# Kernel optimization log

Measured on AMD Instinct MI355X. Metric: run time of the kernel, lower is better.

Reference implementation:

```python
import jax, jax.numpy as jnp
import numpy as np

B, T, N, DIN, D = 8, 20, 1000, 64, 64


def setup_inputs() -> dict:
    key = jax.random.key(0)
    ks = jax.random.split(key, 10)
    stdv = 1.0 / np.sqrt(DIN + D)  # torch reset_param: uniform(-1/sqrt(in_size), ...)
    def gate_w(k):
        return jax.random.uniform(k, (N, DIN + D, D), jnp.float32, -stdv, stdv)
    x = jax.random.normal(ks[0], (B, T, N, DIN), jnp.float32)
    # xavier_normal_ for time_att.W [N, T, D]: fan_in=T*D, fan_out=N*D
    xav_std = np.sqrt(2.0 / (T * D + N * D)).astype(np.float32)
    Wt = jax.random.normal(ks[5], (N, T, D), jnp.float32) * xav_std
    return {
        "x": x,
        "Wi": gate_w(ks[1]), "bi": jnp.zeros((N, D), jnp.float32),
        "Wo": gate_w(ks[2]), "bo": jnp.zeros((N, D), jnp.float32),
        "Wf": gate_w(ks[3]), "bf": jnp.zeros((N, D), jnp.float32),
        "Wc": gate_w(ks[4]), "bc": jnp.zeros((N, D), jnp.float32),
        "Wt": Wt,
    }


def _lstm_att(x, Wi, bi, Wo, bo, Wf, bf, Wc, bc, Wt):
    b, t, n, din = x.shape
    d = Wi.shape[-1]

    def gate(xh, W, bias):
        # per-stock matmul: [b,n,din+d] x [n,din+d,d] -> [b,n,d]
        return jnp.einsum('bni,nio->bno', xh, W) + bias

    def step(carry, xt):
        h, c = carry  # [b,n,d]
        xh = jnp.concatenate([xt, h], axis=-1)
        it = jax.nn.sigmoid(gate(xh, Wi, bi))
        ot = jax.nn.sigmoid(gate(xh, Wo, bo))
        ft = jax.nn.sigmoid(gate(xh, Wf, bf))
        ch = jnp.tanh(gate(xh, Wc, bc))
        c2 = ft * c + it * ch
        h2 = ot * jnp.tanh(c2)
        return (h2, c2), h2

    h0 = jnp.zeros((b, n, d), x.dtype)
    c0 = jnp.zeros((b, n, d), x.dtype)
    xt_seq = jnp.swapaxes(x, 0, 1)  # [t,b,n,din]
    _, hs = jax.lax.scan(step, (h0, c0), xt_seq)
    h = jnp.swapaxes(hs, 0, 1)  # [b,t,n,d] (torch.stack dim=-3)

    # time attention
    h_bntd = jnp.swapaxes(h, 1, 2)  # [b,n,t,d]
    scores = jnp.sum(h_bntd * Wt, axis=-1)  # [b,n,t]
    att = jax.nn.softmax(scores, axis=-1)
    out = jnp.einsum('bnt,bntd->bnd', att, h_bntd)  # matmul([b,n,1,t],[b,n,t,d]).squeeze()
    return out  # [b,n,d]


def reference(x, Wi, bi, Wo, bo, Wf, bf, Wc, bc, Wt):
    return _lstm_att(x, Wi, bi, Wo, bo, Wf, bf, Wc, bc, Wt)
```

## Files before the change

### kernel.cpp

```cpp
#include <hip/hip_runtime.h>

#define TT 20
#define NSTK 1000
#define THREADS 256

typedef float f32x4 __attribute__((ext_vector_type(4)));
typedef _Float16 f16x8 __attribute__((ext_vector_type(8)));
typedef _Float16 f16x2 __attribute__((ext_vector_type(2)));

__device__ __forceinline__ float rcp_f(float x) { return __builtin_amdgcn_rcpf(x); }
__device__ __forceinline__ float sigmoid_f(float x) { return rcp_f(1.0f + __expf(-x)); }
__device__ __forceinline__ float tanh_f(float x) {
    return 1.0f - 2.0f * rcp_f(__expf(2.0f * x) + 1.0f);
}

#define AIDX(kf, q, row, j) ((((kf) * 4 + (q)) * 16 + (row)) * 8 + (j))

extern "C" __global__ void __launch_bounds__(THREADS, 4)
lstm_att_f16(const float* __restrict__ x,
             const float* __restrict__ Wi, const float* __restrict__ bi,
             const float* __restrict__ Wo, const float* __restrict__ bo,
             const float* __restrict__ Wf, const float* __restrict__ bf_,
             const float* __restrict__ Wc, const float* __restrict__ bc,
             const float* __restrict__ Wt,
             float* __restrict__ out)
{
    __shared__ __align__(16) _Float16 afrag[2][2048];
    __shared__ __align__(16) _Float16 hhist[TT * 8 * 64];

    const int n    = blockIdx.x;
    const int tid  = threadIdx.x;
    const int lane = tid & 63;
    const int w    = tid >> 6;
    const int q    = lane >> 4;
    const int r16  = lane & 15;
    const int dcol = w * 16 + r16;
    const bool hi  = lane >= 32;
    const int rowbase = ((lane & 31) >> 4) * 4 + (hi ? 2 : 0);

    f16x8 bw[4][4];
    {
        const float* Wg[4] = {Wi, Wo, Wf, Wc};
        #pragma unroll
        for (int g = 0; g < 4; ++g) {
            const float* base = Wg[g] + (size_t)n * 8192 + dcol;
            #pragma unroll
            for (int kf = 0; kf < 4; ++kf)
                #pragma unroll
                for (int j = 0; j < 8; ++j)
                    bw[g][kf][j] = (_Float16)base[(kf * 32 + q * 8 + j) * 64];
        }
    }
    float biasv[4];
    biasv[0] = bi[n * 64 + dcol];
    biasv[1] = bo[n * 64 + dcol];
    biasv[2] = bf_[n * 64 + dcol];
    biasv[3] = bc[n * 64 + dcol];

    const int sb = tid >> 5, dx = (tid & 31) * 2;
    const int sbase = AIDX(dx >> 5, (dx & 31) >> 3, sb, dx & 7);
    const float* xptr = x + ((size_t)sb * TT * NSTK + (size_t)n) * 64 + dx;

    {
        const float2 x0 = *(const float2*)xptr;
        *(f16x2*)(&afrag[0][sbase]) = (f16x2){(_Float16)x0.x, (_Float16)x0.y};
        #pragma unroll
        for (int u = 0; u < 4; ++u)
            afrag[0][1024 + tid + u * THREADS] = (_Float16)0.0f;
    }
    float2 xreg = *(const float2*)(xptr + (size_t)NSTK * 64);

    float cst0 = 0.f, cst1 = 0.f;

    __syncthreads();

    const int kfh = 2 + (dcol >> 5), kkh = dcol & 31;
    const int hb0 = AIDX(kfh, kkh >> 3, rowbase, kkh & 7);

    for (int t = 0; t < TT; ++t) {
        const int cur = t & 1, nxt = cur ^ 1;

        f16x8 af[4];
        #pragma unroll
        for (int kf = 0; kf < 4; ++kf)
            af[kf] = *(const f16x8*)(&afrag[cur][AIDX(kf, q, r16, 0)]);

        if (t + 1 < TT)
            *(f16x2*)(&afrag[nxt][sbase]) = (f16x2){(_Float16)xreg.x, (_Float16)xreg.y};
        {
            const int tn = (t + 2 < TT) ? t + 2 : TT - 1;
            xreg = *(const float2*)(xptr + (size_t)tn * NSTK * 64);
        }

        f32x4 acc[4];
        #pragma unroll
        for (int g = 0; g < 4; ++g)
            acc[g] = (f32x4){biasv[g], biasv[g], biasv[g], biasv[g]};
        #pragma unroll
        for (int kf = 0; kf < 4; ++kf) {
            #pragma unroll
            for (int g = 0; g < 4; ++g)
                acc[g] = __builtin_amdgcn_mfma_f32_16x16x32_f16(af[kf], bw[g][kf], acc[g], 0, 0, 0);
        }

        float p0[4], p1[4];
        #pragma unroll
        for (int g = 0; g < 4; ++g) {
            const float t2 = __shfl_xor(acc[g][2], 32, 64);
            const float t3 = __shfl_xor(acc[g][3], 32, 64);
            p0[g] = hi ? t2 : acc[g][0];
            p1[g] = hi ? t3 : acc[g][1];
        }

        const float ig0 = sigmoid_f(p0[0]), og0 = sigmoid_f(p0[1]);
        const float fg0 = sigmoid_f(p0[2]), cg0 = tanh_f(p0[3]);
        const float ig1 = sigmoid_f(p1[0]), og1 = sigmoid_f(p1[1]);
        const float fg1 = sigmoid_f(p1[2]), cg1 = tanh_f(p1[3]);
        cst0 = fmaf(fg0, cst0, ig0 * cg0);
        cst1 = fmaf(fg1, cst1, ig1 * cg1);
        const float h0 = og0 * tanh_f(cst0);
        const float h1 = og1 * tanh_f(cst1);

        afrag[nxt][hb0]     = (_Float16)h0;
        afrag[nxt][hb0 + 8] = (_Float16)h1;
        hhist[(t * 8 + rowbase) * 64 + dcol]     = (_Float16)h0;
        hhist[(t * 8 + rowbase + 1) * 64 + dcol] = (_Float16)h1;

        __syncthreads();
    }

    const float* wtg = Wt + (size_t)n * (TT * 64);
    #pragma unroll
    for (int bb = 0; bb < 2; ++bb) {
        const int b = 2 * w + bb;
        float s[TT];
        #pragma unroll
        for (int t = 0; t < TT; ++t)
            s[t] = (float)hhist[(t * 8 + b) * 64 + lane] * wtg[t * 64 + lane];
        #pragma unroll
        for (int t = 0; t < TT; ++t) {
            #pragma unroll
            for (int mk = 32; mk >= 1; mk >>= 1)
                s[t] += __shfl_xor(s[t], mk, 64);
        }
        float m = s[0];
        #pragma unroll
        for (int t = 1; t < TT; ++t) m = fmaxf(m, s[t]);
        float se = 0.f;
        #pragma unroll
        for (int t = 0; t < TT; ++t) { s[t] = __expf(s[t] - m); se += s[t]; }
        const float rs = rcp_f(se);
        float o = 0.f;
        #pragma unroll
        for (int t = 0; t < TT; ++t)
            o = fmaf(s[t], (float)hhist[(t * 8 + b) * 64 + lane], o);
        out[((size_t)b * NSTK + n) * 64 + lane] = o * rs;
    }
}

extern "C" void kernel_launch(void* const* d_in, const int* in_sizes, int n_in,
                              void* d_out, int out_size, void* d_ws, size_t ws_size,
                              hipStream_t stream) {
    const float* x  = (const float*)d_in[0];
    const float* Wi = (const float*)d_in[1];
    const float* bi = (const float*)d_in[2];
    const float* Wo = (const float*)d_in[3];
    const float* bo = (const float*)d_in[4];
    const float* Wf = (const float*)d_in[5];
    const float* bf = (const float*)d_in[6];
    const float* Wc = (const float*)d_in[7];
    const float* bc = (const float*)d_in[8];
    const float* Wt = (const float*)d_in[9];
    float* out = (float*)d_out;

    lstm_att_f16<<<NSTK, THREADS, 0, stream>>>(
        x, Wi, bi, Wo, bo, Wf, bf, Wc, bc, Wt, out);
}
```

Baseline: 56.91 us.

## Split batch across two blocks per stock to double grid parallelism

Launches 2000 blocks instead of 1000, with each block handling 4 of the 8 batch rows for one stock. Each lane now carries one cell state instead of two, which shortens the serial per-step gate math. In exchange, each block loads the full weight set, so weight traffic doubles, and half of the MFMA rows do no useful work. Block indices are interleaved so that both halves of a stock run close together and can share weight data through cache.

New measurement: 138.6 us. 2.43x slower.

```diff
diff --git a/kernel.cpp b/kernel.cpp
--- a/kernel.cpp
+++ b/kernel.cpp
@@ -3,10 +3,10 @@
 #define TT 20
 #define NSTK 1000
 #define THREADS 256
+#define NBLK 2000
 
 typedef float f32x4 __attribute__((ext_vector_type(4)));
 typedef _Float16 f16x8 __attribute__((ext_vector_type(8)));
-typedef _Float16 f16x2 __attribute__((ext_vector_type(2)));
 
 __device__ __forceinline__ float rcp_f(float x) { return __builtin_amdgcn_rcpf(x); }
 __device__ __forceinline__ float sigmoid_f(float x) { return rcp_f(1.0f + __expf(-x)); }
@@ -26,9 +26,12 @@
              float* __restrict__ out)
 {
     __shared__ __align__(16) _Float16 afrag[2][2048];
-    __shared__ __align__(16) _Float16 hhist[TT * 8 * 64];
+    __shared__ __align__(16) _Float16 hhist[TT * 4 * 64];
 
-    const int n    = blockIdx.x;
+    const int idx  = blockIdx.x;
+    const int half = (idx >> 3) & 1;
+    const int n    = ((idx >> 4) << 3) | (idx & 7);
+
     const int tid  = threadIdx.x;
     const int lane = tid & 63;
     const int w    = tid >> 6;
@@ -36,7 +39,9 @@
     const int r16  = lane & 15;
     const int dcol = w * 16 + r16;
     const bool hi  = lane >= 32;
-    const int rowbase = ((lane & 31) >> 4) * 4 + (hi ? 2 : 0);
+    const int g16  = lane >> 4;
+    const int rowh = ((g16 >> 1) & 1) | ((g16 & 1) << 2);
+    const int bbh  = (rowh & 1) | (rowh >> 1);
 
     f16x8 bw[4][4];
     {
@@ -57,25 +62,24 @@
     biasv[2] = bf_[n * 64 + dcol];
     biasv[3] = bc[n * 64 + dcol];
 
-    const int sb = tid >> 5, dx = (tid & 31) * 2;
-    const int sbase = AIDX(dx >> 5, (dx & 31) >> 3, sb, dx & 7);
-    const float* xptr = x + ((size_t)sb * TT * NSTK + (size_t)n) * 64 + dx;
+    const int sb  = tid >> 6;
+    const int dxx = tid & 63;
+    const int rr  = (sb & 1) | ((sb >> 1) << 2);
+    const int sslot = AIDX(dxx >> 5, (dxx & 31) >> 3, rr, dxx & 7);
+    const float* xptr = x + ((size_t)(half * 4 + sb) * TT * NSTK + (size_t)n) * 64 + dxx;
 
-    {
-        const float2 x0 = *(const float2*)xptr;
-        *(f16x2*)(&afrag[0][sbase]) = (f16x2){(_Float16)x0.x, (_Float16)x0.y};
-        #pragma unroll
-        for (int u = 0; u < 4; ++u)
-            afrag[0][1024 + tid + u * THREADS] = (_Float16)0.0f;
-    }
-    float2 xreg = *(const float2*)(xptr + (size_t)NSTK * 64);
+    afrag[0][sslot] = (_Float16)(*xptr);
+    #pragma unroll
+    for (int u = 0; u < 4; ++u)
+        afrag[0][1024 + tid + u * THREADS] = (_Float16)0.0f;
+    float xreg = *(xptr + (size_t)NSTK * 64);
 
-    float cst0 = 0.f, cst1 = 0.f;
+    float cst = 0.f;
 
     __syncthreads();
 
-    const int kfh = 2 + (dcol >> 5), kkh = dcol & 31;
-    const int hb0 = AIDX(kfh, kkh >> 3, rowbase, kkh & 7);
+    const int kkh   = dcol & 31;
+    const int hslot = AIDX(2 + (dcol >> 5), kkh >> 3, rowh, kkh & 7);
 
     for (int t = 0; t < TT; ++t) {
         const int cur = t & 1, nxt = cur ^ 1;
@@ -86,10 +90,10 @@
             af[kf] = *(const f16x8*)(&afrag[cur][AIDX(kf, q, r16, 0)]);
 
         if (t + 1 < TT)
-            *(f16x2*)(&afrag[nxt][sbase]) = (f16x2){(_Float16)xreg.x, (_Float16)xreg.y};
+            afrag[nxt][sslot] = (_Float16)xreg;
         {
             const int tn = (t + 2 < TT) ? t + 2 : TT - 1;
-            xreg = *(const float2*)(xptr + (size_t)tn * NSTK * 64);
+            xreg = *(xptr + (size_t)tn * NSTK * 64);
         }
 
         f32x4 acc[4];
@@ -103,40 +107,30 @@
                 acc[g] = __builtin_amdgcn_mfma_f32_16x16x32_f16(af[kf], bw[g][kf], acc[g], 0, 0, 0);
         }
 
-        float p0[4], p1[4];
+        float pg[4];
         #pragma unroll
         for (int g = 0; g < 4; ++g) {
-            const float t2 = __shfl_xor(acc[g][2], 32, 64);
-            const float t3 = __shfl_xor(acc[g][3], 32, 64);
-            p0[g] = hi ? t2 : acc[g][0];
-            p1[g] = hi ? t3 : acc[g][1];
+            const float t1 = __shfl_xor(acc[g][1], 32, 64);
+            pg[g] = hi ? t1 : acc[g][0];
         }
 
-        const float ig0 = sigmoid_f(p0[0]), og0 = sigmoid_f(p0[1]);
-        const float fg0 = sigmoid_f(p0[2]), cg0 = tanh_f(p0[3]);
-        const float ig1 = sigmoid_f(p1[0]), og1 = sigmoid_f(p1[1]);
-        const float fg1 = sigmoid_f(p1[2]), cg1 = tanh_f(p1[3]);
-        cst0 = fmaf(fg0, cst0, ig0 * cg0);
-        cst1 = fmaf(fg1, cst1, ig1 * cg1);
-        const float h0 = og0 * tanh_f(cst0);
-        const float h1 = og1 * tanh_f(cst1);
+        const float ig = sigmoid_f(pg[0]), og = sigmoid_f(pg[1]);
+        const float fg = sigmoid_f(pg[2]), cg = tanh_f(pg[3]);
+        cst = fmaf(fg, cst, ig * cg);
+        const float hv = og * tanh_f(cst);
 
-        afrag[nxt][hb0]     = (_Float16)h0;
-        afrag[nxt][hb0 + 8] = (_Float16)h1;
-        hhist[(t * 8 + rowbase) * 64 + dcol]     = (_Float16)h0;
-        hhist[(t * 8 + rowbase + 1) * 64 + dcol] = (_Float16)h1;
+        afrag[nxt][hslot] = (_Float16)hv;
+        hhist[(t * 4 + bbh) * 64 + dcol] = (_Float16)hv;
 
         __syncthreads();
     }
 
     const float* wtg = Wt + (size_t)n * (TT * 64);
-    #pragma unroll
-    for (int bb = 0; bb < 2; ++bb) {
-        const int b = 2 * w + bb;
+    {
         float s[TT];
         #pragma unroll
         for (int t = 0; t < TT; ++t)
-            s[t] = (float)hhist[(t * 8 + b) * 64 + lane] * wtg[t * 64 + lane];
+            s[t] = (float)hhist[(t * 4 + w) * 64 + lane] * wtg[t * 64 + lane];
         #pragma unroll
         for (int t = 0; t < TT; ++t) {
             #pragma unroll
@@ -153,8 +147,8 @@
         float o = 0.f;
         #pragma unroll
         for (int t = 0; t < TT; ++t)
-            o = fmaf(s[t], (float)hhist[(t * 8 + b) * 64 + lane], o);
-        out[((size_t)b * NSTK + n) * 64 + lane] = o * rs;
+            o = fmaf(s[t], (float)hhist[(t * 4 + w) * 64 + lane], o);
+        out[((size_t)(half * 4 + w) * NSTK + n) * 64 + lane] = o * rs;
     }
 }
 
@@ -173,6 +167,6 @@
     const float* Wt = (const float*)d_in[9];
     float* out = (float*)d_out;
 
-    lstm_att_f16<<<NSTK, THREADS, 0, stream>>>(
+    lstm_att_f16<<<NBLK, THREADS, 0, stream>>>(
         x, Wi, bi, Wo, bo, Wf, bf, Wc, bc, Wt, out);
 }
```

## Stage gate weights through LDS with coalesced loads and prescale for exp2

Applied to the files above, without the earlier changes.

Gate weights are now loaded as coalesced float4 chunks into a double-buffered LDS staging area, replacing the strided per-column global loads. The shared memory is enlarged to 32 KB and aliased with afrag/hhist. Weights and biases are also prescaled by log2(e) (or 2·log2(e) for tanh), so the sigmoid and tanh activations can call exp2 directly without a multiply. The larger LDS footprint may lower occupancy, and the 16 extra barriers add cost to the prologue.

Measured after the change: 74.84 us. 31.5% more time.

```diff
diff --git a/kernel.cpp b/kernel.cpp
--- a/kernel.cpp
+++ b/kernel.cpp
@@ -4,15 +4,15 @@
 #define NSTK 1000
 #define THREADS 256
 
+#define SC_SIG  1.44269504089f
+#define SC_TANH 2.88539008178f
+
 typedef float f32x4 __attribute__((ext_vector_type(4)));
 typedef _Float16 f16x8 __attribute__((ext_vector_type(8)));
 typedef _Float16 f16x2 __attribute__((ext_vector_type(2)));
 
 __device__ __forceinline__ float rcp_f(float x) { return __builtin_amdgcn_rcpf(x); }
-__device__ __forceinline__ float sigmoid_f(float x) { return rcp_f(1.0f + __expf(-x)); }
-__device__ __forceinline__ float tanh_f(float x) {
-    return 1.0f - 2.0f * rcp_f(__expf(2.0f * x) + 1.0f);
-}
+__device__ __forceinline__ float exp2_f(float x) { return __builtin_amdgcn_exp2f(x); }
 
 #define AIDX(kf, q, row, j) ((((kf) * 4 + (q)) * 16 + (row)) * 8 + (j))
 
@@ -25,8 +25,9 @@
              const float* __restrict__ Wt,
              float* __restrict__ out)
 {
-    __shared__ __align__(16) _Float16 afrag[2][2048];
-    __shared__ __align__(16) _Float16 hhist[TT * 8 * 64];
+    __shared__ __align__(16) char smem[32768];
+    _Float16 (*afrag)[2048] = (_Float16 (*)[2048])smem;
+    _Float16* hhist = (_Float16*)(smem + 8192);
 
     const int n    = blockIdx.x;
     const int tid  = threadIdx.x;
@@ -41,21 +42,42 @@
     f16x8 bw[4][4];
     {
         const float* Wg[4] = {Wi, Wo, Wf, Wc};
-        #pragma unroll
-        for (int g = 0; g < 4; ++g) {
-            const float* base = Wg[g] + (size_t)n * 8192 + dcol;
-            #pragma unroll
-            for (int kf = 0; kf < 4; ++kf)
+        float4* wst[2] = { (float4*)smem, (float4*)(smem + 16384) };
+        float4 reg[4];
+        {
+            const float4* src = (const float4*)(Wg[0] + (size_t)n * 8192);
+            #pragma unroll
+            for (int u = 0; u < 4; ++u) reg[u] = src[u * 256 + tid];
+        }
+        #pragma unroll
+        for (int c = 0; c < 8; ++c) {
+            const int g = c >> 1, hf = c & 1, buf = c & 1;
+            float4* wb = wst[buf];
+            #pragma unroll
+            for (int u = 0; u < 4; ++u) wb[u * 256 + tid] = reg[u];
+            if (c + 1 < 8) {
+                const int g2 = (c + 1) >> 1, hf2 = (c + 1) & 1;
+                const float4* src = (const float4*)(Wg[g2] + (size_t)n * 8192 + hf2 * 4096);
+                #pragma unroll
+                for (int u = 0; u < 4; ++u) reg[u] = src[u * 256 + tid];
+            }
+            __syncthreads();
+            const float* wf = (const float*)wst[buf];
+            const float sc = (g == 3) ? SC_TANH : SC_SIG;
+            #pragma unroll
+            for (int kfl = 0; kfl < 2; ++kfl)
                 #pragma unroll
                 for (int j = 0; j < 8; ++j)
-                    bw[g][kf][j] = (_Float16)base[(kf * 32 + q * 8 + j) * 64];
+                    bw[g][hf * 2 + kfl][j] =
+                        (_Float16)(wf[(kfl * 32 + q * 8 + j) * 64 + dcol] * sc);
+            __syncthreads();
         }
     }
     float biasv[4];
-    biasv[0] = bi[n * 64 + dcol];
-    biasv[1] = bo[n * 64 + dcol];
-    biasv[2] = bf_[n * 64 + dcol];
-    biasv[3] = bc[n * 64 + dcol];
+    biasv[0] = bi[n * 64 + dcol]  * SC_SIG;
+    biasv[1] = bo[n * 64 + dcol]  * SC_SIG;
+    biasv[2] = bf_[n * 64 + dcol] * SC_SIG;
+    biasv[3] = bc[n * 64 + dcol]  * SC_TANH;
 
     const int sb = tid >> 5, dx = (tid & 31) * 2;
     const int sbase = AIDX(dx >> 5, (dx & 31) >> 3, sb, dx & 7);
@@ -112,14 +134,20 @@
             p1[g] = hi ? t3 : acc[g][1];
         }
 
-        const float ig0 = sigmoid_f(p0[0]), og0 = sigmoid_f(p0[1]);
-        const float fg0 = sigmoid_f(p0[2]), cg0 = tanh_f(p0[3]);
-        const float ig1 = sigmoid_f(p1[0]), og1 = sigmoid_f(p1[1]);
-        const float fg1 = sigmoid_f(p1[2]), cg1 = tanh_f(p1[3]);
+        const float ig0 = rcp_f(1.0f + exp2_f(-p0[0]));
+        const float og0 = rcp_f(1.0f + exp2_f(-p0[1]));
+        const float fg0 = rcp_f(1.0f + exp2_f(-p0[2]));
+        const float cg0 = 1.0f - 2.0f * rcp_f(exp2_f(p0[3]) + 1.0f);
+        const float ig1 = rcp_f(1.0f + exp2_f(-p1[0]));
+        const float og1 = rcp_f(1.0f + exp2_f(-p1[1]));
+        const float fg1 = rcp_f(1.0f + exp2_f(-p1[2]));
+        const float cg1 = 1.0f - 2.0f * rcp_f(exp2_f(p1[3]) + 1.0f);
         cst0 = fmaf(fg0, cst0, ig0 * cg0);
         cst1 = fmaf(fg1, cst1, ig1 * cg1);
-        const float h0 = og0 * tanh_f(cst0);
-        const float h1 = og1 * tanh_f(cst1);
+        const float th0 = 1.0f - 2.0f * rcp_f(exp2_f(cst0 * SC_TANH) + 1.0f);
+        const float th1 = 1.0f - 2.0f * rcp_f(exp2_f(cst1 * SC_TANH) + 1.0f);
+        const float h0 = og0 * th0;
+        const float h1 = og1 * th1;
 
         afrag[nxt][hb0]     = (_Float16)h0;
         afrag[nxt][hb0 + 8] = (_Float16)h1;
@@ -148,7 +176,7 @@
         for (int t = 1; t < TT; ++t) m = fmaxf(m, s[t]);
         float se = 0.f;
         #pragma unroll
-        for (int t = 0; t < TT; ++t) { s[t] = __expf(s[t] - m); se += s[t]; }
+        for (int t = 0; t < TT; ++t) { s[t] = exp2_f((s[t] - m) * SC_SIG); se += s[t]; }
         const float rs = rcp_f(se);
         float o = 0.f;
         #pragma unroll
```

## Process two stocks per block and fold exp2 scaling into weights

Applied to the files above, without the earlier changes.

Each block now runs the LSTM recurrence for two stocks at once, interleaving their independent MFMA chains and activation math so each per-step barrier and its latency are shared between two recurrences. The grid halves to 500 blocks and launch bounds drop to two blocks per SM to make room for the doubled weight registers. Weights and biases are prescaled by log2(e) (and 2·log2(e) for the tanh gate) so the activations use raw exp2 instead of expf. The cost is fewer blocks (less parallelism across the 256 CUs), higher register pressure, and small extra rounding from scaling before the fp16 conversion.

Result: slower. 60.97 us (+7.1%).

```diff
diff --git a/kernel.cpp b/kernel.cpp
--- a/kernel.cpp
+++ b/kernel.cpp
@@ -3,32 +3,35 @@
 #define TT 20
 #define NSTK 1000
 #define THREADS 256
+#define NBLK 500
+
+#define SC_SIG  1.44269504089f
+#define SC_TANH 2.88539008178f
 
 typedef float f32x4 __attribute__((ext_vector_type(4)));
 typedef _Float16 f16x8 __attribute__((ext_vector_type(8)));
 typedef _Float16 f16x2 __attribute__((ext_vector_type(2)));
 
 __device__ __forceinline__ float rcp_f(float x) { return __builtin_amdgcn_rcpf(x); }
-__device__ __forceinline__ float sigmoid_f(float x) { return rcp_f(1.0f + __expf(-x)); }
-__device__ __forceinline__ float tanh_f(float x) {
-    return 1.0f - 2.0f * rcp_f(__expf(2.0f * x) + 1.0f);
-}
+__device__ __forceinline__ float exp2_f(float x) { return __builtin_amdgcn_exp2f(x); }
 
 #define AIDX(kf, q, row, j) ((((kf) * 4 + (q)) * 16 + (row)) * 8 + (j))
 
-extern "C" __global__ void __launch_bounds__(THREADS, 4)
-lstm_att_f16(const float* __restrict__ x,
-             const float* __restrict__ Wi, const float* __restrict__ bi,
-             const float* __restrict__ Wo, const float* __restrict__ bo,
-             const float* __restrict__ Wf, const float* __restrict__ bf_,
-             const float* __restrict__ Wc, const float* __restrict__ bc,
-             const float* __restrict__ Wt,
-             float* __restrict__ out)
+extern "C" __global__ void __launch_bounds__(THREADS, 2)
+lstm_att_2stk(const float* __restrict__ x,
+              const float* __restrict__ Wi, const float* __restrict__ bi,
+              const float* __restrict__ Wo, const float* __restrict__ bo,
+              const float* __restrict__ Wf, const float* __restrict__ bf_,
+              const float* __restrict__ Wc, const float* __restrict__ bc,
+              const float* __restrict__ Wt,
+              float* __restrict__ out)
 {
-    __shared__ __align__(16) _Float16 afrag[2][2048];
-    __shared__ __align__(16) _Float16 hhist[TT * 8 * 64];
-
-    const int n    = blockIdx.x;
+    __shared__ __align__(16) _Float16 afragA[2][2048];
+    __shared__ __align__(16) _Float16 afragB[2][2048];
+    __shared__ __align__(16) _Float16 hhistA[TT * 8 * 64];
+    __shared__ __align__(16) _Float16 hhistB[TT * 8 * 64];
+
+    const int n0   = blockIdx.x * 2;
     const int tid  = threadIdx.x;
     const int lane = tid & 63;
     const int w    = tid >> 6;
@@ -38,39 +41,49 @@
     const bool hi  = lane >= 32;
     const int rowbase = ((lane & 31) >> 4) * 4 + (hi ? 2 : 0);
 
-    f16x8 bw[4][4];
+    f16x8 bwA[4][4], bwB[4][4];
+    float biasA[4], biasB[4];
     {
         const float* Wg[4] = {Wi, Wo, Wf, Wc};
+        const float* Bg[4] = {bi, bo, bf_, bc};
         #pragma unroll
         for (int g = 0; g < 4; ++g) {
-            const float* base = Wg[g] + (size_t)n * 8192 + dcol;
+            const float sc = (g == 3) ? SC_TANH : SC_SIG;
+            const float* baseA = Wg[g] + (size_t)n0 * 8192 + dcol;
+            const float* baseB = baseA + 8192;
             #pragma unroll
             for (int kf = 0; kf < 4; ++kf)
                 #pragma unroll
-                for (int j = 0; j < 8; ++j)
-                    bw[g][kf][j] = (_Float16)base[(kf * 32 + q * 8 + j) * 64];
-        }
-    }
-    float biasv[4];
-    biasv[0] = bi[n * 64 + dcol];
-    biasv[1] = bo[n * 64 + dcol];
-    biasv[2] = bf_[n * 64 + dcol];
-    biasv[3] = bc[n * 64 + dcol];
+                for (int j = 0; j < 8; ++j) {
+                    const int off = (kf * 32 + q * 8 + j) * 64;
+                    bwA[g][kf][j] = (_Float16)(baseA[off] * sc);
+                    bwB[g][kf][j] = (_Float16)(baseB[off] * sc);
+                }
+            biasA[g] = Bg[g][n0 * 64 + dcol] * sc;
+            biasB[g] = Bg[g][(n0 + 1) * 64 + dcol] * sc;
+        }
+    }
 
     const int sb = tid >> 5, dx = (tid & 31) * 2;
     const int sbase = AIDX(dx >> 5, (dx & 31) >> 3, sb, dx & 7);
-    const float* xptr = x + ((size_t)sb * TT * NSTK + (size_t)n) * 64 + dx;
+    const float* xptrA = x + ((size_t)sb * TT * NSTK + n0) * 64 + dx;
+    const float* xptrB = xptrA + 64;
 
     {
-        const float2 x0 = *(const float2*)xptr;
-        *(f16x2*)(&afrag[0][sbase]) = (f16x2){(_Float16)x0.x, (_Float16)x0.y};
-        #pragma unroll
-        for (int u = 0; u < 4; ++u)
-            afrag[0][1024 + tid + u * THREADS] = (_Float16)0.0f;
-    }
-    float2 xreg = *(const float2*)(xptr + (size_t)NSTK * 64);
-
-    float cst0 = 0.f, cst1 = 0.f;
+        const float2 a0 = *(const float2*)xptrA;
+        const float2 b0 = *(const float2*)xptrB;
+        *(f16x2*)(&afragA[0][sbase]) = (f16x2){(_Float16)a0.x, (_Float16)a0.y};
+        *(f16x2*)(&afragB[0][sbase]) = (f16x2){(_Float16)b0.x, (_Float16)b0.y};
+    }
+    #pragma unroll
+    for (int u = 0; u < 4; ++u) {
+        afragA[0][1024 + tid + u * THREADS] = (_Float16)0.0f;
+        afragB[0][1024 + tid + u * THREADS] = (_Float16)0.0f;
+    }
+    float2 xregA = *(const float2*)(xptrA + (size_t)NSTK * 64);
+    float2 xregB = *(const float2*)(xptrB + (size_t)NSTK * 64);
+
+    float cA0 = 0.f, cA1 = 0.f, cB0 = 0.f, cB1 = 0.f;
 
     __syncthreads();
 
@@ -80,81 +93,126 @@
     for (int t = 0; t < TT; ++t) {
         const int cur = t & 1, nxt = cur ^ 1;
 
-        f16x8 af[4];
-        #pragma unroll
-        for (int kf = 0; kf < 4; ++kf)
-            af[kf] = *(const f16x8*)(&afrag[cur][AIDX(kf, q, r16, 0)]);
-
-        if (t + 1 < TT)
-            *(f16x2*)(&afrag[nxt][sbase]) = (f16x2){(_Float16)xreg.x, (_Float16)xreg.y};
+        f16x8 afA[4], afB[4];
+        #pragma unroll
+        for (int kf = 0; kf < 4; ++kf) {
+            afA[kf] = *(const f16x8*)(&afragA[cur][AIDX(kf, q, r16, 0)]);
+            afB[kf] = *(const f16x8*)(&afragB[cur][AIDX(kf, q, r16, 0)]);
+        }
+
+        if (t + 1 < TT) {
+            *(f16x2*)(&afragA[nxt][sbase]) = (f16x2){(_Float16)xregA.x, (_Float16)xregA.y};
+            *(f16x2*)(&afragB[nxt][sbase]) = (f16x2){(_Float16)xregB.x, (_Float16)xregB.y};
+        }
         {
-            const int tn = (t + 2 < TT) ? t + 2 : TT - 1;
-            xreg = *(const float2*)(xptr + (size_t)tn * NSTK * 64);
-        }
-
-        f32x4 acc[4];
-        #pragma unroll
-        for (int g = 0; g < 4; ++g)
-            acc[g] = (f32x4){biasv[g], biasv[g], biasv[g], biasv[g]};
+            const size_t off = (size_t)((t + 2 < TT) ? t + 2 : TT - 1) * (NSTK * 64);
+            xregA = *(const float2*)(xptrA + off);
+            xregB = *(const float2*)(xptrB + off);
+        }
+
+        f32x4 accA[4], accB[4];
+        #pragma unroll
+        for (int g = 0; g < 4; ++g) {
+            accA[g] = (f32x4){biasA[g], biasA[g], biasA[g], biasA[g]};
+            accB[g] = (f32x4){biasB[g], biasB[g], biasB[g], biasB[g]};
+        }
         #pragma unroll
         for (int kf = 0; kf < 4; ++kf) {
             #pragma unroll
-            for (int g = 0; g < 4; ++g)
-                acc[g] = __builtin_amdgcn_mfma_f32_16x16x32_f16(af[kf], bw[g][kf], acc[g], 0, 0, 0);
-        }
-
-        float p0[4], p1[4];
+            for (int g = 0; g < 4; ++g) {
+                accA[g] = __builtin_amdgcn_mfma_f32_16x16x32_f16(afA[kf], bwA[g][kf], accA[g], 0, 0, 0);
+                accB[g] = __builtin_amdgcn_mfma_f32_16x16x32_f16(afB[kf], bwB[g][kf], accB[g], 0, 0, 0);
+            }
+        }
+
+        float pA0[4], pA1[4], pB0[4], pB1[4];
         #pragma unroll
         for (int g = 0; g < 4; ++g) {
-            const float t2 = __shfl_xor(acc[g][2], 32, 64);
-            const float t3 = __shfl_xor(acc[g][3], 32, 64);
-            p0[g] = hi ? t2 : acc[g][0];
-            p1[g] = hi ? t3 : acc[g][1];
-        }
-
-        const float ig0 = sigmoid_f(p0[0]), og0 = sigmoid_f(p0[1]);
-        const float fg0 = sigmoid_f(p0[2]), cg0 = tanh_f(p0[3]);
-        const float ig1 = sigmoid_f(p1[0]), og1 = sigmoid_f(p1[1]);
-        const float fg1 = sigmoid_f(p1[2]), cg1 = tanh_f(p1[3]);
-        cst0 = fmaf(fg0, cst0, ig0 * cg0);
-        cst1 = fmaf(fg1, cst1, ig1 * cg1);
-        const float h0 = og0 * tanh_f(cst0);
-        const float h1 = og1 * tanh_f(cst1);
-
-        afrag[nxt][hb0]     = (_Float16)h0;
-        afrag[nxt][hb0 + 8] = (_Float16)h1;
-        hhist[(t * 8 + rowbase) * 64 + dcol]     = (_Float16)h0;
-        hhist[(t * 8 + rowbase + 1) * 64 + dcol] = (_Float16)h1;
+            const float a2 = __shfl_xor(accA[g][2], 32, 64);
+            const float a3 = __shfl_xor(accA[g][3], 32, 64);
+            const float b2 = __shfl_xor(accB[g][2], 32, 64);
+            const float b3 = __shfl_xor(accB[g][3], 32, 64);
+            pA0[g] = hi ? a2 : accA[g][0];
+            pA1[g] = hi ? a3 : accA[g][1];
+            pB0[g] = hi ? b2 : accB[g][0];
+            pB1[g] = hi ? b3 : accB[g][1];
+        }
+
+        const float igA0 = rcp_f(1.0f + exp2_f(-pA0[0]));
+        const float ogA0 = rcp_f(1.0f + exp2_f(-pA0[1]));
+        const float fgA0 = rcp_f(1.0f + exp2_f(-pA0[2]));
+        const float cgA0 = 1.0f - 2.0f * rcp_f(exp2_f(pA0[3]) + 1.0f);
+        const float igA1 = rcp_f(1.0f + exp2_f(-pA1[0]));
+        const float ogA1 = rcp_f(1.0f + exp2_f(-pA1[1]));
+        const float fgA1 = rcp_f(1.0f + exp2_f(-pA1[2]));
+        const float cgA1 = 1.0f - 2.0f * rcp_f(exp2_f(pA1[3]) + 1.0f);
+        const float igB0 = rcp_f(1.0f + exp2_f(-pB0[0]));
+        const float ogB0 = rcp_f(1.0f + exp2_f(-pB0[1]));
+        const float fgB0 = rcp_f(1.0f + exp2_f(-pB0[2]));
+        const float cgB0 = 1.0f - 2.0f * rcp_f(exp2_f(pB0[3]) + 1.0f);
+        const float igB1 = rcp_f(1.0f + exp2_f(-pB1[0]));
+        const float ogB1 = rcp_f(1.0f + exp2_f(-pB1[1]));
+        const float fgB1 = rcp_f(1.0f + exp2_f(-pB1[2]));
+        const float cgB1 = 1.0f - 2.0f * rcp_f(exp2_f(pB1[3]) + 1.0f);
+
+        cA0 = fmaf(fgA0, cA0, igA0 * cgA0);
+        cA1 = fmaf(fgA1, cA1, igA1 * cgA1);
+        cB0 = fmaf(fgB0, cB0, igB0 * cgB0);
+        cB1 = fmaf(fgB1, cB1, igB1 * cgB1);
+        const float hA0 = ogA0 * (1.0f - 2.0f * rcp_f(exp2_f(cA0 * SC_TANH) + 1.0f));
+        const float hA1 = ogA1 * (1.0f - 2.0f * rcp_f(exp2_f(cA1 * SC_TANH) + 1.0f));
+        const float hB0 = ogB0 * (1.0f - 2.0f * rcp_f(exp2_f(cB0 * SC_TANH) + 1.0f));
+        const float hB1 = ogB1 * (1.0f - 2.0f * rcp_f(exp2_f(cB1 * SC_TANH) + 1.0f));
+
+        afragA[nxt][hb0]     = (_Float16)hA0;
+        afragA[nxt][hb0 + 8] = (_Float16)hA1;
+        afragB[nxt][hb0]     = (_Float16)hB0;
+        afragB[nxt][hb0 + 8] = (_Float16)hB1;
+        hhistA[(t * 8 + rowbase) * 64 + dcol]     = (_Float16)hA0;
+        hhistA[(t * 8 + rowbase + 1) * 64 + dcol] = (_Float16)hA1;
+        hhistB[(t * 8 + rowbase) * 64 + dcol]     = (_Float16)hB0;
+        hhistB[(t * 8 + rowbase + 1) * 64 + dcol] = (_Float16)hB1;
 
         __syncthreads();
     }
 
-    const float* wtg = Wt + (size_t)n * (TT * 64);
+    const float* wtgA = Wt + (size_t)n0 * (TT * 64);
+    const float* wtgB = wtgA + TT * 64;
     #pragma unroll
     for (int bb = 0; bb < 2; ++bb) {
         const int b = 2 * w + bb;
-        float s[TT];
-        #pragma unroll
-        for (int t = 0; t < TT; ++t)
-            s[t] = (float)hhist[(t * 8 + b) * 64 + lane] * wtg[t * 64 + lane];
+        float sA[TT], sB[TT];
+        #pragma unroll
+        for (int t = 0; t < TT; ++t) {
+            sA[t] = (float)hhistA[(t * 8 + b) * 64 + lane] * wtgA[t * 64 + lane];
+            sB[t] = (float)hhistB[(t * 8 + b) * 64 + lane] * wtgB[t * 64 + lane];
+        }
         #pragma unroll
         for (int t = 0; t < TT; ++t) {
             #pragma unroll
-            for (int mk = 32; mk >= 1; mk >>= 1)
-                s[t] += __shfl_xor(s[t], mk, 64);
-        }
-        float m = s[0];
-        #pragma unroll
-        for (int t = 1; t < TT; ++t) m = fmaxf(m, s[t]);
-        float se = 0.f;
-        #pragma unroll
-        for (int t = 0; t < TT; ++t) { s[t] = __expf(s[t] - m); se += s[t]; }
-        const float rs = rcp_f(se);
-        float o = 0.f;
-        #pragma unroll
-        for (int t = 0; t < TT; ++t)
-            o = fmaf(s[t], (float)hhist[(t * 8 + b) * 64 + lane], o);
-        out[((size_t)b * NSTK + n) * 64 + lane] = o * rs;
+            for (int mk = 32; mk >= 1; mk >>= 1) {
+                sA[t] += __shfl_xor(sA[t], mk, 64);
+                sB[t] += __shfl_xor(sB[t], mk, 64);
+            }
+        }
+        float mA = sA[0], mB = sB[0];
+        #pragma unroll
+        for (int t = 1; t < TT; ++t) { mA = fmaxf(mA, sA[t]); mB = fmaxf(mB, sB[t]); }
+        float seA = 0.f, seB = 0.f;
+        #pragma unroll
+        for (int t = 0; t < TT; ++t) {
+            sA[t] = exp2_f((sA[t] - mA) * SC_SIG); seA += sA[t];
+            sB[t] = exp2_f((sB[t] - mB) * SC_SIG); seB += sB[t];
+        }
+        const float rsA = rcp_f(seA), rsB = rcp_f(seB);
+        float oA = 0.f, oB = 0.f;
+        #pragma unroll
+        for (int t = 0; t < TT; ++t) {
+            oA = fmaf(sA[t], (float)hhistA[(t * 8 + b) * 64 + lane], oA);
+            oB = fmaf(sB[t], (float)hhistB[(t * 8 + b) * 64 + lane], oB);
+        }
+        out[((size_t)b * NSTK + n0) * 64 + lane]     = oA * rsA;
+        out[((size_t)b * NSTK + n0 + 1) * 64 + lane] = oB * rsB;
     }
 }
 
@@ -173,6 +231,6 @@
     const float* Wt = (const float*)d_in[9];
     float* out = (float*)d_out;
 
-    lstm_att_f16<<<NSTK, THREADS, 0, stream>>>(
+    lstm_att_2stk<<<NBLK, THREADS, 0, stream>>>(
         x, Wi, bi, Wo, bo, Wf, bf, Wc, bc, Wt, out);
 }
```
